# Kernel optimization log

Hardware: AMD Instinct MI355X
Metric: run time of the kernel (lower is better)

The kernel has to match this reference:

```python
import math
import jax, jax.numpy as jnp
import numpy as np

B, N, H, NH, DD, L = 4, 384, 256, 8, 32, 4
HD = H // NH
V = 11           # num_species + 1 (padding row 0)
CUTOFF = 5.0

def _ln(x, g, b):
    m = jnp.mean(x, axis=-1, keepdims=True)
    v = jnp.mean(jnp.square(x - m), axis=-1, keepdims=True)
    return (x - m) / jnp.sqrt(v + 1e-5) * g + b

def setup_inputs() -> dict:
    key = jax.random.key(0)
    ks = iter(jax.random.split(key, 64))
    def nrm(shape, s=0.05):
        return jax.random.normal(next(ks), shape, jnp.float32) * s
    return {
        'node_indices': jax.random.randint(next(ks), (B, N), 0, V),
        'positions': jax.random.normal(next(ks), (B, N, 3), jnp.float32),
        'mask': jnp.ones((B, N), jnp.float32),
        'emb': nrm((V, H)).at[0].set(0.0),
        'ln1_g': jnp.ones((L, H)), 'ln1_b': jnp.zeros((L, H)),
        'qkv_w': nrm((L, H, 3 * H)), 'qkv_b': jnp.zeros((L, 3 * H)),
        'out_w': nrm((L, H, H)), 'out_b': jnp.zeros((L, H)),
        'rb_w1': nrm((L, DD, H)), 'rb_b1': jnp.zeros((L, H)),
        'rb_w2': nrm((L, H, NH)), 'rb_b2': jnp.zeros((L, NH)),
        'gate_w1': nrm((L, H, H)), 'gate_b1': jnp.zeros((L, H)),
        'gate_w2': nrm((L, H, H)), 'gate_b2': jnp.zeros((L, H)),
        'ln2_g': jnp.ones((L, H)), 'ln2_b': jnp.zeros((L, H)),
        'ff_w1': nrm((L, H, 2 * H)), 'ff_b1': jnp.zeros((L, 2 * H)),
        'ff_w2': nrm((L, 2 * H, H)), 'ff_b2': jnp.zeros((L, H)),
        'pool_g': jnp.ones((H,)), 'pool_beta': jnp.zeros((H,)),
        'pool_w': nrm((H, H)), 'pool_b': jnp.zeros((H,)),
        'eh_w': nrm((H, 1)), 'eh_b': jnp.zeros((1,)),
    }

def _forward(node_indices, positions, mask, emb, ln1_g, ln1_b, qkv_w, qkv_b,
             out_w, out_b, rb_w1, rb_b1, rb_w2, rb_b2, gate_w1, gate_b1,
             gate_w2, gate_b2, ln2_g, ln2_b, ff_w1, ff_b1, ff_w2, ff_b2,
             pool_g, pool_beta, pool_w, pool_b, eh_w, eh_b):
    mask_b = mask > 0
    x = emb[node_indices] * mask_b[..., None]               # [B,N,H]
    pos = positions * mask_b[..., None].astype(positions.dtype)
    rel = pos[:, :, None, :] - pos[:, None, :, :]           # [B,N,N,3]
    dist = jnp.linalg.norm(rel + 1e-9, axis=-1)             # [B,N,N]
    adj = (dist <= CUTOFF).astype(jnp.float32)
    adj = adj * mask_b[:, None, :] * mask_b[:, :, None]
    edge = adj > 0
    isolated = mask_b & ~edge.any(axis=-1)
    adj = adj + isolated.astype(jnp.float32)[:, :, None] * jnp.eye(N, dtype=jnp.float32)
    edge = adj > 0
    # Bessel envelope features [B,N,N,DD]
    kk = jnp.arange(1, DD + 1, dtype=jnp.float32)
    ang = math.pi * kk * (dist / CUTOFF)[..., None]
    feat = jnp.sin(ang) / (dist[..., None] + 1e-6)
    feat = feat * (dist <= CUTOFF)[..., None].astype(jnp.float32)
    feat = feat * adj[..., None]

    scale = math.sqrt(HD)
    NEG = jnp.finfo(jnp.float32).min
    for l in range(L):
        res = x
        h = _ln(x, ln1_g[l], ln1_b[l])
        qkv = h @ qkv_w[l] + qkv_b[l]
        q, k, v = jnp.split(qkv, 3, axis=-1)
        q = q.reshape(B, N, NH, HD)
        k = k.reshape(B, N, NH, HD)
        v = v.reshape(B, N, NH, HD)
        logits = jnp.einsum('bihd,bjhd->bhij', q, k) / scale
        hb = jax.nn.silu(feat @ rb_w1[l] + rb_b1[l])        # [B,N,N,H]
        bias = hb @ rb_w2[l] + rb_b2[l]                     # [B,N,N,NH]
        logits = logits + bias.transpose(0, 3, 1, 2)
        logits = jnp.where(edge[:, None, :, :], logits, NEG)
        attn = jax.nn.softmax(logits, axis=-1)
        ctx = jnp.einsum('bhij,bjhd->bihd', attn, v).reshape(B, N, H)
        gated = jax.nn.silu(h @ gate_w1[l] + gate_b1[l]) @ gate_w2[l] + gate_b2[l]
        x = res + ((ctx * jax.nn.sigmoid(gated)) @ out_w[l] + out_b[l])
        y = _ln(x, ln2_g[l], ln2_b[l])
        x = x + (jax.nn.gelu(y @ ff_w1[l] + ff_b1[l], approximate=False) @ ff_w2[l] + ff_b2[l])

    pooled = jax.nn.silu(_ln(x, pool_g, pool_beta) @ pool_w + pool_b)
    masked = pooled * mask_b[..., None]
    counts = jnp.maximum(jnp.sum(mask_b, axis=1), 1)
    graph = jnp.sum(masked, axis=1) / counts[:, None]
    energy = (graph @ eh_w + eh_b)[:, 0]                    # [B]
    return energy

def reference(node_indices, positions, mask, emb, ln1_g, ln1_b, qkv_w, qkv_b,
              out_w, out_b, rb_w1, rb_b1, rb_w2, rb_b2, gate_w1, gate_b1,
              gate_w2, gate_b2, ln2_g, ln2_b, ff_w1, ff_b1, ff_w2, ff_b2,
              pool_g, pool_beta, pool_w, pool_b, eh_w, eh_b):
    return _forward(node_indices, positions, mask, emb, ln1_g, ln1_b, qkv_w,
                    qkv_b, out_w, out_b, rb_w1, rb_b1, rb_w2, rb_b2, gate_w1,
                    gate_b1, gate_w2, gate_b2, ln2_g, ln2_b, ff_w1, ff_b1,
                    ff_w2, ff_b2, pool_g, pool_beta, pool_w, pool_b, eh_w, eh_b)
```

## Files before the change

kernel.cpp:

```cpp
#include <hip/hip_runtime.h>
#include <hip/hip_bf16.h>
#include <math.h>

constexpr int B_ = 4, N_ = 384, H_ = 256, NH_ = 8, DD_ = 32, L_ = 4;
constexpr int M_ = B_ * N_;
constexpr float CUT = 5.0f;
constexpr float PI_ = 3.14159265358979323846f;
constexpr float INVSC = 0.17677669529663687f;
constexpr int TBL_N = 4096;
constexpr int TBL_STRIDE = 4098;

typedef __attribute__((ext_vector_type(8))) short short8;
typedef __attribute__((ext_vector_type(4))) float f32x4;
typedef __attribute__((ext_vector_type(4))) unsigned short u16x4;
using u16 = unsigned short;

__device__ __forceinline__ u16 f2b(float f) {
  __hip_bfloat16 h = __float2bfloat16(f);
  return *reinterpret_cast<u16*>(&h);
}
__device__ __forceinline__ float b2f(u16 u) {
  __hip_bfloat16 h;
  *reinterpret_cast<u16*>(&h) = u;
  return __bfloat162float(h);
}

__device__ __forceinline__ float wave_sum(float v) {
#pragma unroll
  for (int s = 1; s < 64; s <<= 1) v += __shfl_xor(v, s);
  return v;
}


__device__ __forceinline__ void bias_item(const float* __restrict__ pos,
                                          const float* __restrict__ mask,
                                          const float* __restrict__ tbl2,
                                          u16* __restrict__ biasb, int e) {
  int j = e % N_;
  int t = e / N_;
  int i = t % N_;
  int b = t / N_;
  float mi = mask[b * N_ + i], mj = mask[b * N_ + j];
  const float* pi = pos + (size_t)(b * N_ + i) * 3;
  const float* pj = pos + (size_t)(b * N_ + j) * 3;
  float dx = pi[0] - pj[0] + 1e-9f;
  float dy = pi[1] - pj[1] + 1e-9f;
  float dz = pi[2] - pj[2] + 1e-9f;
  float d = sqrtf(dx * dx + dy * dy + dz * dz);
  bool edge = (mi > 0.f && mj > 0.f) && (d <= CUT);
  size_t plane = (size_t)N_ * N_;
  size_t obase = (size_t)b * NH_ * plane + (size_t)i * N_ + j;
  size_t lstride = (size_t)B_ * NH_ * plane;
  if (edge) {
    int ixrow;
    float fr;
    if (i == j) {
      ixrow = TBL_N + 1;
      fr = 0.f;
    } else {
      float u = d * ((float)TBL_N / CUT);
      int ix = (int)u;
      ix = ix > TBL_N - 1 ? TBL_N - 1 : ix;
      fr = u - (float)ix;
      ixrow = ix;
    }
    const float4* r0 = (const float4*)(tbl2 + (size_t)ixrow * 32);
    const float4* r1 = (const float4*)(tbl2 + (size_t)(ixrow + 1) * 32);
    float4 a0[8], a1[8];
#pragma unroll
    for (int q = 0; q < 8; q++) {
      a0[q] = r0[q];
      a1[q] = r1[q];
    }
    float w0 = 1.f - fr;
#pragma unroll
    for (int q = 0; q < 8; q++) {
      float v0[4] = {a0[q].x, a0[q].y, a0[q].z, a0[q].w};
      float v1[4] = {a1[q].x, a1[q].y, a1[q].z, a1[q].w};
#pragma unroll
      for (int c = 0; c < 4; c++) {
        int lh = q * 4 + c;
        int l = lh >> 3, h = lh & 7;
        float v = v0[c] * w0 + v1[c] * fr;
        biasb[(size_t)l * lstride + obase + (size_t)h * plane] = f2b(v);
      }
    }
  } else {
#pragma unroll
    for (int lh = 0; lh < 32; lh++) {
      int l = lh >> 3, h = lh & 7;
      biasb[(size_t)l * lstride + obase + (size_t)h * plane] = 0xFF80;
    }
  }
}

struct TrJob {
  const float* src;
  u16* dst;
  int K, N, nx, ny, nz, base, dstride;
};
struct TrJobs {
  TrJob j[7];
};
__global__ __launch_bounds__(256) void setup_all_k(TrJobs jobs,
                                                   const float* __restrict__ rb_w1,
                                                   const float* __restrict__ rb_b1,
                                                   const float* __restrict__ rb_w2,
                                                   const float* __restrict__ rb_b2,
                                                   float* __restrict__ tbl2,
                                                   const int* __restrict__ nidx,
                                                   const float* __restrict__ mask,
                                                   const float* __restrict__ emb,
                                                   float* __restrict__ X) {
  __shared__ float sfA[64][32];
  __shared__ float hbA[64][260];
  __shared__ float t[32][33];
  int bid = blockIdx.x;
  int tid = threadIdx.x;
  if (bid < 260) {
    constexpr int TT = 64;
    int l = bid / 65;
    int t0 = (bid % 65) * TT;
#pragma unroll
    for (int m = 0; m < 8; m++) {
      int idx = m * 256 + tid;
      int tl = idx >> 5, k = idx & 31;
      int tt = t0 + tl;
      float d = (tt <= TBL_N) ? (tt * (CUT / (float)TBL_N)) : 1.7320508075688772e-9f;
      float ang = PI_ * (k + 1) * d * (1.f / CUT);
      sfA[tl][k] = sinf(ang) / (d + 1e-6f);
    }
    __syncthreads();
    float w1c[32];
    const float* w1 = rb_w1 + (size_t)l * DD_ * H_;
#pragma unroll
    for (int k = 0; k < 32; k++) w1c[k] = w1[k * H_ + tid];
    float b1v = rb_b1[l * H_ + tid];
    for (int tl = 0; tl < TT; tl++) {
      float pre = b1v;
      const float4* sfp = (const float4*)sfA[tl];
#pragma unroll
      for (int kq = 0; kq < 8; kq++) {
        float4 s4 = sfp[kq];
        pre += s4.x * w1c[kq * 4] + s4.y * w1c[kq * 4 + 1] + s4.z * w1c[kq * 4 + 2] +
               s4.w * w1c[kq * 4 + 3];
      }
      hbA[tl][tid] = pre / (1.f + __expf(-pre));
    }
    __syncthreads();
    const float* w2 = rb_w2 + (size_t)l * H_ * NH_;
    int o = tid & 7;
    float b2v = rb_b2[l * NH_ + o];
#pragma unroll
    for (int half = 0; half < 2; half++) {
      int tl = (tid >> 3) + half * 32;
      float acc = b2v;
      const float4* hp = (const float4*)hbA[tl];
#pragma unroll 4
      for (int hq = 0; hq < 64; hq++) {
        float4 h4 = hp[hq];
        acc += h4.x * w2[(hq * 4 + 0) * NH_ + o] + h4.y * w2[(hq * 4 + 1) * NH_ + o] +
               h4.z * w2[(hq * 4 + 2) * NH_ + o] + h4.w * w2[(hq * 4 + 3) * NH_ + o];
      }
      int tt = t0 + tl;
      if (tt <= TBL_STRIDE) tbl2[(size_t)tt * 32 + l * NH_ + o] = acc;
    }
  } else if (bid < 2884) {
    int tb = bid - 260;
    int ji = 0;
#pragma unroll
    for (int q = 1; q < 7; q++)
      if (tb >= jobs.j[q].base) ji = q;
    const TrJob& J = jobs.j[ji];
    int local = tb - J.base;
    int z = local / (J.nx * J.ny);
    int r2 = local % (J.nx * J.ny);
    int ky = r2 / J.nx, kx = r2 % J.nx;
    int n0 = kx * 32, k0 = ky * 32;
    const float* s = J.src + (size_t)z * J.K * J.N;
    u16* d = J.dst + (size_t)z * J.dstride;
    int r = tid >> 3, c4 = (tid & 7) * 4;
    float4 v = *(const float4*)(s + (size_t)(k0 + r) * J.N + n0 + c4);
    t[r][c4 + 0] = v.x;
    t[r][c4 + 1] = v.y;
    t[r][c4 + 2] = v.z;
    t[r][c4 + 3] = v.w;
    __syncthreads();
    u16x4 o;
    o[0] = f2b(t[c4 + 0][r]);
    o[1] = f2b(t[c4 + 1][r]);
    o[2] = f2b(t[c4 + 2][r]);
    o[3] = f2b(t[c4 + 3][r]);
    *(u16x4*)(d + (size_t)(n0 + r) * J.K + k0 + c4) = o;
  } else {
    int e = (bid - 2884) * 256 + tid;
    int mrow = e >> 8, c = e & 255;
    float mb = mask[mrow] > 0.f ? 1.f : 0.f;
    X[e] = emb[nidx[mrow] * H_ + c] * mb;
  }
}

__global__ __launch_bounds__(256) void ln_k(const float* __restrict__ X,
                                            const float* __restrict__ g,
                                            const float* __restrict__ bta,
                                            u16* __restrict__ O) {
  int wave = threadIdx.x >> 6, lane = threadIdx.x & 63;
  int row = blockIdx.x * 4 + wave;
  const float* xr = X + (size_t)row * H_;
  float4 v = *(const float4*)(xr + lane * 4);
  float s = v.x + v.y + v.z + v.w;
  s = wave_sum(s);
  float m = s * (1.f / H_);
  float dx = v.x - m, dy = v.y - m, dz = v.z - m, dw = v.w - m;
  float vs = dx * dx + dy * dy + dz * dz + dw * dw;
  vs = wave_sum(vs);
  float rs = rsqrtf(vs * (1.f / H_) + 1e-5f);
  float4 gg = *(const float4*)(g + lane * 4);
  float4 bb = *(const float4*)(bta + lane * 4);
  u16x4 o;
  o[0] = f2b(dx * rs * gg.x + bb.x);
  o[1] = f2b(dy * rs * gg.y + bb.y);
  o[2] = f2b(dz * rs * gg.z + bb.z);
  o[3] = f2b(dw * rs * gg.w + bb.w);
  *(u16x4*)(O + (size_t)row * H_ + lane * 4) = o;
}

template <int ACT, bool RES, bool PRE, bool OBF>
__device__ __forceinline__ void mgemm_body(u16* __restrict__ As, u16* __restrict__ Bs,
                                           const void* __restrict__ Av,
                                           const u16* __restrict__ WT,
                                           const float* __restrict__ bias,
                                           const float* __restrict__ resid,
                                           void* __restrict__ Cv, int K, int Nc,
                                           int lda, const float* __restrict__ G,
                                           const float* __restrict__ bias2,
                                           int m0, int n0) {
  const int tid = threadIdx.x;
  const int wave = tid >> 6, lane = tid & 63;
  const int wr = wave >> 1, wc = wave & 1, lr = lane & 15, lg = lane >> 4;
  f32x4 acc[2][2] = {};
  const int srow = tid >> 2, sp = tid & 3;
  for (int k0 = 0; k0 < K; k0 += 128) {
#pragma unroll
    for (int s4 = 0; s4 < 4; s4++) {
      int s = sp * 4 + s4;
      int phys = s ^ (srow & 15);
      if (PRE) {
        const float* ap = (const float*)Av + (size_t)(m0 + srow) * lda + k0 + s * 8;
        const float* gp = G + (size_t)(m0 + srow) * lda + k0 + s * 8;
        float4 a0 = *(const float4*)ap;
        float4 a1 = *(const float4*)(ap + 4);
        float4 g0 = *(const float4*)gp;
        float4 g1 = *(const float4*)(gp + 4);
        short8 vv;
        vv[0] = (short)f2b(a0.x / (1.f + __expf(-g0.x)));
        vv[1] = (short)f2b(a0.y / (1.f + __expf(-g0.y)));
        vv[2] = (short)f2b(a0.z / (1.f + __expf(-g0.z)));
        vv[3] = (short)f2b(a0.w / (1.f + __expf(-g0.w)));
        vv[4] = (short)f2b(a1.x / (1.f + __expf(-g1.x)));
        vv[5] = (short)f2b(a1.y / (1.f + __expf(-g1.y)));
        vv[6] = (short)f2b(a1.z / (1.f + __expf(-g1.z)));
        vv[7] = (short)f2b(a1.w / (1.f + __expf(-g1.w)));
        *(short8*)&As[srow * 128 + phys * 8] = vv;
      } else {
        const u16* Ab = (const u16*)Av;
        short8 v = *(const short8*)(Ab + (size_t)(m0 + srow) * lda + k0 + s * 8);
        *(short8*)&As[srow * 128 + phys * 8] = v;
      }
      short8 w = *(const short8*)(WT + (size_t)(n0 + srow) * K + k0 + s * 8);
      *(short8*)&Bs[srow * 128 + phys * 8] = w;
    }
    __syncthreads();
#pragma unroll
    for (int kk = 0; kk < 4; kk++) {
      int slot = kk * 4 + lg;
      short8 af[2], bf_[2];
#pragma unroll
      for (int i = 0; i < 2; i++) {
        int row = wr * 32 + i * 16 + lr;
        af[i] = *(const short8*)&As[row * 128 + (slot ^ (row & 15)) * 8];
      }
#pragma unroll
      for (int j = 0; j < 2; j++) {
        int row = wc * 32 + j * 16 + lr;
        bf_[j] = *(const short8*)&Bs[row * 128 + (slot ^ (row & 15)) * 8];
      }
#pragma unroll
      for (int i = 0; i < 2; i++)
#pragma unroll
        for (int j = 0; j < 2; j++)
          acc[i][j] = __builtin_amdgcn_mfma_f32_16x16x32_bf16(af[i], bf_[j], acc[i][j], 0, 0, 0);
    }
    __syncthreads();
  }
#pragma unroll
  for (int i = 0; i < 2; i++)
#pragma unroll
    for (int j = 0; j < 2; j++)
#pragma unroll
      for (int rg = 0; rg < 4; rg++) {
        int row = m0 + wr * 32 + i * 16 + lg * 4 + rg;
        int col = n0 + wc * 32 + j * 16 + lr;
        float v;
        if (ACT == 3) {
          float bv = (col < 768) ? bias[col] : bias2[col - 768];
          v = acc[i][j][rg] + bv;
          if (col >= 768) v = v / (1.f + __expf(-v));
        } else {
          v = acc[i][j][rg] + bias[col];
          if (ACT == 1) v = v / (1.f + __expf(-v));
          if (ACT == 2) v = 0.5f * v * (1.f + erff(v * 0.70710678118654752f));
        }
        if (RES) v += resid[(size_t)row * Nc + col];
        if (OBF)
          ((u16*)Cv)[(size_t)row * Nc + col] = f2b(v);
        else
          ((float*)Cv)[(size_t)row * Nc + col] = v;
      }
}

template <int ACT, bool RES, bool PRE, bool OBF>
__global__ __launch_bounds__(256) void mgemm_k(const void* __restrict__ Av,
                                               const u16* __restrict__ WT,
                                               const float* __restrict__ bias,
                                               const float* __restrict__ resid,
                                               void* __restrict__ Cv, int K, int Nc,
                                               int lda, const float* __restrict__ G,
                                               const float* __restrict__ bias2) {
  __shared__ u16 As[64 * 128];
  __shared__ u16 Bs[64 * 128];
  mgemm_body<ACT, RES, PRE, OBF>(As, Bs, Av, WT, bias, resid, Cv, K, Nc, lda, G, bias2,
                                 blockIdx.y * 64, blockIdx.x * 64);
}

__global__ __launch_bounds__(256) void qkv_bias_k(const u16* __restrict__ hb,
                                                  const u16* __restrict__ wqg,
                                                  const float* __restrict__ qb,
                                                  const float* __restrict__ gb1,
                                                  u16* __restrict__ qgb,
                                                  const float* __restrict__ pos,
                                                  const float* __restrict__ mask,
                                                  const float* __restrict__ tbl2,
                                                  u16* __restrict__ biasb) {
  __shared__ u16 As[64 * 128];
  __shared__ u16 Bs[64 * 128];
  int bid = blockIdx.x;
  if (bid < 384) {
    mgemm_body<3, false, false, true>(As, Bs, hb, wqg, qb, nullptr, qgb, 256, 1024, 256,
                                      nullptr, gb1, (bid >> 4) * 64, (bid & 15) * 64);
  } else {
    bias_item(pos, mask, tbl2, biasb, (bid - 384) * 256 + threadIdx.x);
  }
}

__device__ __forceinline__ void attn_body(u16* __restrict__ FragQ, u16* __restrict__ FragK,
                                          u16* __restrict__ FragV, float* __restrict__ smax,
                                          float* __restrict__ ssum,
                                          const u16* __restrict__ qkv,
                                          const u16* __restrict__ biasb,
                                          float* __restrict__ ctx, int qs,
                                          int it, int hh, int b) {
  u16* FragP = FragK;
  float* pbuf = (float*)FragV;
  const int i0 = it * 32;
  const int tid = threadIdx.x;
  const size_t bb = (size_t)b * N_;

  if (tid < 128) {
    int q = tid >> 2, dc = tid & 3;
    short8 v = *(const short8*)(qkv + (bb + i0 + q) * qs + hh * 32 + dc * 8);
    *(short8*)&FragQ[(((q >> 4) * 64) + (q & 15) + 16 * dc) * 8] = v;
  }
#pragma unroll
  for (int m = 0; m < 6; m++) {
    int idx = m * 256 + tid;
    int key = idx >> 2, dc = idx & 3;
    const u16* kb = qkv + (bb + key) * qs + 256 + hh * 32 + dc * 8;
    short8 kv = *(const short8*)kb;
    *(short8*)&FragK[(((key >> 4) * 64) + (key & 15) + 16 * dc) * 8] = kv;
    short8 vv = *(const short8*)(kb + 256);
    int kc = key >> 5, sub = (key >> 3) & 3, kj = key & 7;
#pragma unroll
    for (int j = 0; j < 8; j++) {
      int d = dc * 8 + j;
      FragV[(((kc * 2 + (d >> 4)) * 64) + (d & 15) + 16 * sub) * 8 + kj] = (u16)vv[j];
    }
  }
  __syncthreads();

  const int wave = tid >> 6, lane = tid & 63;
  const int rh = wave & 1, kh = wave >> 1;
  const int g = lane >> 4, c = lane & 15;
  const u16* bptr = biasb + (size_t)(b * NH_ + hh) * N_ * N_;

  short8 qf = *(const short8*)&FragQ[(rh * 64 + lane) * 8];
  f32x4 sc[12];
#pragma unroll
  for (int t = 0; t < 12; t++) {
    int T = kh * 12 + t;
    short8 kf = *(const short8*)&FragK[(T * 64 + lane) * 8];
    f32x4 z = {0.f, 0.f, 0.f, 0.f};
    sc[t] = __builtin_amdgcn_mfma_f32_16x16x32_bf16(qf, kf, z, 0, 0, 0);
    int key = 16 * T + c;
#pragma unroll
    for (int reg = 0; reg < 4; reg++) {
      int row = i0 + 16 * rh + 4 * g + reg;
      float bv = b2f(bptr[(size_t)row * N_ + key]);
      sc[t][reg] = sc[t][reg] * INVSC + bv;
    }
  }
  float mx[4];
#pragma unroll
  for (int reg = 0; reg < 4; reg++) {
    float m = sc[0][reg];
#pragma unroll
    for (int t = 1; t < 12; t++) m = fmaxf(m, sc[t][reg]);
#pragma unroll
    for (int s = 1; s < 16; s <<= 1) m = fmaxf(m, __shfl_xor(m, s));
    mx[reg] = m;
  }
  if (c == 0) {
#pragma unroll
    for (int reg = 0; reg < 4; reg++) smax[kh * 32 + 16 * rh + 4 * g + reg] = mx[reg];
  }
  __syncthreads();
  float sm[4];
#pragma unroll
  for (int reg = 0; reg < 4; reg++) {
    float M = fmaxf(smax[16 * rh + 4 * g + reg], smax[32 + 16 * rh + 4 * g + reg]);
    float s = 0.f;
#pragma unroll
    for (int t = 0; t < 12; t++) {
      float p = __expf(sc[t][reg] - M);
      sc[t][reg] = p;
      s += p;
    }
    sm[reg] = s;
  }
#pragma unroll
  for (int reg = 0; reg < 4; reg++) {
#pragma unroll
    for (int s = 1; s < 16; s <<= 1) sm[reg] += __shfl_xor(sm[reg], s);
  }
  if (c == 0) {
#pragma unroll
    for (int reg = 0; reg < 4; reg++) ssum[kh * 32 + 16 * rh + 4 * g + reg] = sm[reg];
  }
#pragma unroll
  for (int t = 0; t < 12; t++) {
    int T = kh * 12 + t;
    int kc = T >> 1;
    int sub = (2 * T + (c >> 3)) & 3;
#pragma unroll
    for (int reg = 0; reg < 4; reg++) {
      FragP[((rh * 12 + kc) * 64 + (4 * g + reg) + 16 * sub) * 8 + (c & 7)] =
          f2b(sc[t][reg]);
    }
  }
  __syncthreads();
  float Ls[4];
#pragma unroll
  for (int reg = 0; reg < 4; reg++)
    Ls[reg] = ssum[16 * rh + 4 * g + reg] + ssum[32 + 16 * rh + 4 * g + reg];

  f32x4 pcc[2] = {};
#pragma unroll
  for (int t = 0; t < 6; t++) {
    int kc = kh * 6 + t;
    short8 pf = *(const short8*)&FragP[((rh * 12 + kc) * 64 + lane) * 8];
#pragma unroll
    for (int nh = 0; nh < 2; nh++) {
      short8 vf = *(const short8*)&FragV[((kc * 2 + nh) * 64 + lane) * 8];
      pcc[nh] = __builtin_amdgcn_mfma_f32_16x16x32_bf16(pf, vf, pcc[nh], 0, 0, 0);
    }
  }
  __syncthreads();
  if (kh == 1) {
#pragma unroll
    for (int nh = 0; nh < 2; nh++)
#pragma unroll
      for (int reg = 0; reg < 4; reg++)
        pbuf[rh * 512 + (4 * g + reg) * 32 + nh * 16 + c] = pcc[nh][reg];
  }
  __syncthreads();
  if (kh == 0) {
#pragma unroll
    for (int nh = 0; nh < 2; nh++)
#pragma unroll
      for (int reg = 0; reg < 4; reg++) {
        float v = pcc[nh][reg] + pbuf[rh * 512 + (4 * g + reg) * 32 + nh * 16 + c];
        int row = i0 + 16 * rh + 4 * g + reg;
        ctx[(bb + row) * H_ + hh * 32 + nh * 16 + c] = v / Ls[reg];
      }
  }
}

__global__ __launch_bounds__(256) void attn_g2_k(const u16* __restrict__ qkv,
                                                 const u16* __restrict__ biasb,
                                                 float* __restrict__ ctx,
                                                 const u16* __restrict__ wg2,
                                                 const float* __restrict__ gb2,
                                                 float* __restrict__ g2) {
  __shared__ __align__(16) u16 SMEM[(2 + 24 + 24) * 64 * 8];
  __shared__ float sred[2 * 32 * 2];
  int bid = blockIdx.x;
  if (bid < 384) {
    int it = bid % 12;
    int t = bid / 12;
    attn_body(SMEM, SMEM + 1024, SMEM + 1024 + 12288, sred, sred + 64,
              qkv, biasb, ctx, 1024, it, t % NH_, t / NH_);
  } else {
    int g = bid - 384;
    mgemm_body<0, false, false, false>(SMEM, SMEM + 8192, (const void*)(qkv + 768), wg2,
                                       gb2, nullptr, g2, 256, 256, 1024, nullptr,
                                       nullptr, (g >> 2) * 64, (g & 3) * 64);
  }
}

__global__ __launch_bounds__(256) void energy_k(const float* __restrict__ p2,
                                                const float* __restrict__ mask,
                                                const float* __restrict__ ehw,
                                                const float* __restrict__ ehb,
                                                float* __restrict__ out) {
  int b = blockIdx.x, h = threadIdx.x;
  float s = 0.f, cnt = 0.f;
#pragma unroll 4
  for (int i = 0; i < N_; i++) {
    float m = mask[b * N_ + i] > 0.f ? 1.f : 0.f;
    s += p2[(size_t)(b * N_ + i) * H_ + h] * m;
    cnt += m;
  }
  float val = s * ehw[h];
  __shared__ float red[256];
  red[h] = val;
  __syncthreads();
  for (int st = 128; st > 0; st >>= 1) {
    if (h < st) red[h] += red[h + st];
    __syncthreads();
  }
  if (h == 0) {
    float c = cnt < 1.f ? 1.f : cnt;
    out[b] = red[0] / c + ehb[0];
  }
}

extern "C" void kernel_launch(void* const* d_in, const int* in_sizes, int n_in,
                              void* d_out, int out_size, void* d_ws, size_t ws_size,
                              hipStream_t stream) {
  const int* node_idx = (const int*)d_in[0];
  const float* positions = (const float*)d_in[1];
  const float* mask = (const float*)d_in[2];
  const float* emb = (const float*)d_in[3];
  const float* ln1_g = (const float*)d_in[4];
  const float* ln1_b = (const float*)d_in[5];
  const float* qkv_w = (const float*)d_in[6];
  const float* qkv_b = (const float*)d_in[7];
  const float* out_w = (const float*)d_in[8];
  const float* out_b = (const float*)d_in[9];
  const float* rb_w1 = (const float*)d_in[10];
  const float* rb_b1 = (const float*)d_in[11];
  const float* rb_w2 = (const float*)d_in[12];
  const float* rb_b2 = (const float*)d_in[13];
  const float* gate_w1 = (const float*)d_in[14];
  const float* gate_b1 = (const float*)d_in[15];
  const float* gate_w2 = (const float*)d_in[16];
  const float* gate_b2 = (const float*)d_in[17];
  const float* ln2_g = (const float*)d_in[18];
  const float* ln2_b = (const float*)d_in[19];
  const float* ff_w1 = (const float*)d_in[20];
  const float* ff_b1 = (const float*)d_in[21];
  const float* ff_w2 = (const float*)d_in[22];
  const float* ff_b2 = (const float*)d_in[23];
  const float* pool_g = (const float*)d_in[24];
  const float* pool_beta = (const float*)d_in[25];
  const float* pool_w = (const float*)d_in[26];
  const float* pool_b = (const float*)d_in[27];
  const float* eh_w = (const float*)d_in[28];
  const float* eh_b = (const float*)d_in[29];
  float* eout = (float*)d_out;

  char* W8 = (char*)d_ws;
  float* x = (float*)(W8 + 0);
  u16* qgb = (u16*)(W8 + 1572864);
  float* ctx = (float*)(W8 + 4718592);
  float* g2 = (float*)(W8 + 6291456);
  u16* hb = (u16*)(W8 + 7864320);
  u16* ffb = (u16*)(W8 + 8650752);
  float* tbl2 = (float*)(W8 + 12582912);
  u16* wt = (u16*)(W8 + 13631488);
  u16* wt_qg = wt;
  u16* wt_out = wt + 1048576;
  u16* wt_g2 = wt + 1310720;
  u16* wt_f1 = wt + 1572864;
  u16* wt_f2 = wt + 2097152;
  u16* wt_p = wt + 2621440;
  u16* biasb = (u16*)(W8 + 19005440);
  const size_t bias_lstride = (size_t)B_ * NH_ * N_ * N_;

  {
    TrJobs jobs;
    jobs.j[0] = {qkv_w, wt_qg, 256, 768, 24, 8, 4, 0, 262144};
    jobs.j[1] = {gate_w1, wt_qg + 768 * 256, 256, 256, 8, 8, 4, 768, 262144};
    jobs.j[2] = {out_w, wt_out, 256, 256, 8, 8, 4, 1024, 65536};
    jobs.j[3] = {gate_w2, wt_g2, 256, 256, 8, 8, 4, 1280, 65536};
    jobs.j[4] = {ff_w1, wt_f1, 256, 512, 16, 8, 4, 1536, 131072};
    jobs.j[5] = {ff_w2, wt_f2, 512, 256, 8, 16, 4, 2048, 131072};
    jobs.j[6] = {pool_w, wt_p, 256, 256, 8, 8, 1, 2560, 65536};
    setup_all_k<<<4420, 256, 0, stream>>>(jobs, rb_w1, rb_b1, rb_w2, rb_b2, tbl2,
                                          node_idx, mask, emb, x);
  }

  for (int l = 0; l < L_; l++) {
    const float* qb = qkv_b + (size_t)l * 3 * H_;
    const float* ob = out_b + (size_t)l * H_;
    const float* gb1 = gate_b1 + (size_t)l * H_;
    const float* gb2 = gate_b2 + (size_t)l * H_;
    const float* fb1 = ff_b1 + (size_t)l * 2 * H_;
    const float* fb2 = ff_b2 + (size_t)l * H_;
    u16* wqg = wt_qg + (size_t)l * 1024 * 256;
    u16* wo = wt_out + (size_t)l * 256 * 256;
    u16* wg2 = wt_g2 + (size_t)l * 256 * 256;
    u16* wf1 = wt_f1 + (size_t)l * 512 * 256;
    u16* wf2 = wt_f2 + (size_t)l * 256 * 512;

    ln_k<<<M_ / 4, 256, 0, stream>>>(x, ln1_g + l * H_, ln1_b + l * H_, hb);
    if (l == 0) {
      qkv_bias_k<<<2688, 256, 0, stream>>>(hb, wqg, qb, gb1, qgb, positions, mask, tbl2,
                                           biasb);
    } else {
      mgemm_k<3, false, false, true><<<dim3(16, 24), 256, 0, stream>>>(
          hb, wqg, qb, nullptr, qgb, 256, 1024, 256, nullptr, gb1);
    }
    attn_g2_k<<<480, 256, 0, stream>>>(qgb, biasb + (size_t)l * bias_lstride, ctx,
                                       wg2, gb2, g2);
    mgemm_k<0, true, true, false><<<dim3(4, 24), 256, 0, stream>>>(
        ctx, wo, ob, x, x, 256, 256, 256, g2, nullptr);
    ln_k<<<M_ / 4, 256, 0, stream>>>(x, ln2_g + l * H_, ln2_b + l * H_, hb);
    mgemm_k<2, false, false, true><<<dim3(8, 24), 256, 0, stream>>>(
        hb, wf1, fb1, nullptr, ffb, 256, 512, 256, nullptr, nullptr);
    mgemm_k<0, true, false, false><<<dim3(4, 24), 256, 0, stream>>>(
        ffb, wf2, fb2, x, x, 512, 256, 512, nullptr, nullptr);
  }

  ln_k<<<M_ / 4, 256, 0, stream>>>(x, pool_g, pool_beta, hb);
  mgemm_k<1, false, false, false><<<dim3(4, 24), 256, 0, stream>>>(
      hb, wt_p, pool_b, nullptr, ctx, 256, 256, 256, nullptr, nullptr);
  energy_k<<<B_, 256, 0, stream>>>(ctx, mask, eh_w, eh_b, eout);
}
```

Before: 275.9 us.

## Fuse LayerNorm into residual GEMM epilogues and embedding setup

Removes the standalone LayerNorm kernels. The first LN is folded into the embedding branch of the setup kernel. Each later LN runs in the epilogue of a new full-row GEMM kernel (64 rows × 256 cols per block) that handles the out-projection and FF2 residual updates. This saves several launches and a re-read of x per layer. In exchange, these GEMMs now launch only 24 blocks instead of 96, which cuts parallelism on a large GPU. Variance is computed as E[x²]−mean² in one pass, which is less numerically stable than the two-pass form.

```diff
diff --git a/kernel.cpp b/kernel.cpp
--- a/kernel.cpp
+++ b/kernel.cpp
@@ -111,10 +111,14 @@
                                                    const int* __restrict__ nidx,
                                                    const float* __restrict__ mask,
                                                    const float* __restrict__ emb,
-                                                   float* __restrict__ X) {
+                                                   float* __restrict__ X,
+                                                   const float* __restrict__ l1g,
+                                                   const float* __restrict__ l1b,
+                                                   u16* __restrict__ HB) {
   __shared__ float sfA[64][32];
   __shared__ float hbA[64][260];
   __shared__ float t[32][33];
+  __shared__ float sw[8];
   int bid = blockIdx.x;
   int tid = threadIdx.x;
   if (bid < 260) {
@@ -193,36 +197,24 @@
     o[3] = f2b(t[c4 + 3][r]);
     *(u16x4*)(d + (size_t)(n0 + r) * J.K + k0 + c4) = o;
   } else {
-    int e = (bid - 2884) * 256 + tid;
-    int mrow = e >> 8, c = e & 255;
-    float mb = mask[mrow] > 0.f ? 1.f : 0.f;
-    X[e] = emb[nidx[mrow] * H_ + c] * mb;
-  }
-}
-
-__global__ __launch_bounds__(256) void ln_k(const float* __restrict__ X,
-                                            const float* __restrict__ g,
-                                            const float* __restrict__ bta,
-                                            u16* __restrict__ O) {
-  int wave = threadIdx.x >> 6, lane = threadIdx.x & 63;
-  int row = blockIdx.x * 4 + wave;
-  const float* xr = X + (size_t)row * H_;
-  float4 v = *(const float4*)(xr + lane * 4);
-  float s = v.x + v.y + v.z + v.w;
-  s = wave_sum(s);
-  float m = s * (1.f / H_);
-  float dx = v.x - m, dy = v.y - m, dz = v.z - m, dw = v.w - m;
-  float vs = dx * dx + dy * dy + dz * dz + dw * dw;
-  vs = wave_sum(vs);
-  float rs = rsqrtf(vs * (1.f / H_) + 1e-5f);
-  float4 gg = *(const float4*)(g + lane * 4);
-  float4 bb = *(const float4*)(bta + lane * 4);
-  u16x4 o;
-  o[0] = f2b(dx * rs * gg.x + bb.x);
-  o[1] = f2b(dy * rs * gg.y + bb.y);
-  o[2] = f2b(dz * rs * gg.z + bb.z);
-  o[3] = f2b(dw * rs * gg.w + bb.w);
-  *(u16x4*)(O + (size_t)row * H_ + lane * 4) = o;
+    int row = bid - 2884;
+    float mb = mask[row] > 0.f ? 1.f : 0.f;
+    float v = emb[nidx[row] * H_ + tid] * mb;
+    X[(size_t)row * H_ + tid] = v;
+    float s = wave_sum(v);
+    float q = wave_sum(v * v);
+    int wv = tid >> 6, ln = tid & 63;
+    if (ln == 0) {
+      sw[wv] = s;
+      sw[4 + wv] = q;
+    }
+    __syncthreads();
+    float ts = sw[0] + sw[1] + sw[2] + sw[3];
+    float tq = sw[4] + sw[5] + sw[6] + sw[7];
+    float m = ts * (1.f / 256.f);
+    float rs = rsqrtf(tq * (1.f / 256.f) - m * m + 1e-5f);
+    HB[(size_t)row * H_ + tid] = f2b((v - m) * rs * l1g[tid] + l1b[tid]);
+  }
 }
 
 template <int ACT, bool RES, bool PRE, bool OBF>
@@ -331,6 +323,114 @@
   __shared__ u16 Bs[64 * 128];
   mgemm_body<ACT, RES, PRE, OBF>(As, Bs, Av, WT, bias, resid, Cv, K, Nc, lda, G, bias2,
                                  blockIdx.y * 64, blockIdx.x * 64);
+}
+
+template <bool PRE>
+__global__ __launch_bounds__(256) void glngemm_k(const void* __restrict__ Av,
+                                                 const u16* __restrict__ WT,
+                                                 const float* __restrict__ bias,
+                                                 const float* __restrict__ G,
+                                                 float* __restrict__ Xio,
+                                                 u16* __restrict__ hb,
+                                                 const float* __restrict__ lng,
+                                                 const float* __restrict__ lnb,
+                                                 int K, int lda) {
+  __shared__ u16 As[64 * 64];
+  __shared__ u16 Bs[256 * 64];
+  const int m0 = blockIdx.x * 64;
+  const int tid = threadIdx.x;
+  const int wave = tid >> 6, lane = tid & 63;
+  const int lr = lane & 15, lg = lane >> 4;
+  f32x4 acc[16] = {};
+  const int srow = tid >> 2, sp = tid & 3;
+  for (int k0 = 0; k0 < K; k0 += 64) {
+#pragma unroll
+    for (int s2 = 0; s2 < 2; s2++) {
+      int s = sp * 2 + s2;
+      int phys = s ^ (srow & 7);
+      if (PRE) {
+        const float* ap = (const float*)Av + (size_t)(m0 + srow) * lda + k0 + s * 8;
+        const float* gp = G + (size_t)(m0 + srow) * lda + k0 + s * 8;
+        short8 vv;
+#pragma unroll
+        for (int q = 0; q < 8; q++) {
+          vv[q] = (short)f2b(ap[q] / (1.f + __expf(-gp[q])));
+        }
+        *(short8*)&As[srow * 64 + phys * 8] = vv;
+      } else {
+        short8 v = *(const short8*)((const u16*)Av + (size_t)(m0 + srow) * lda + k0 + s * 8);
+        *(short8*)&As[srow * 64 + phys * 8] = v;
+      }
+    }
+    {
+      const u16* wr_ = WT + (size_t)tid * K + k0;
+#pragma unroll
+      for (int s = 0; s < 8; s++) {
+        int phys = s ^ (tid & 7);
+        *(short8*)&Bs[tid * 64 + phys * 8] = *(const short8*)(wr_ + s * 8);
+      }
+    }
+    __syncthreads();
+#pragma unroll
+    for (int grp = 0; grp < 2; grp++) {
+      int arow = wave * 16 + lr;
+      int achunk = (grp * 4 + lg) ^ (arow & 7);
+      short8 af = *(const short8*)&As[arow * 64 + achunk * 8];
+#pragma unroll
+      for (int t = 0; t < 16; t++) {
+        int brow = t * 16 + lr;
+        int bchunk = (grp * 4 + lg) ^ (brow & 7);
+        short8 bf = *(const short8*)&Bs[brow * 64 + bchunk * 8];
+        acc[t] = __builtin_amdgcn_mfma_f32_16x16x32_bf16(af, bf, acc[t], 0, 0, 0);
+      }
+    }
+    __syncthreads();
+  }
+#pragma unroll
+  for (int t = 0; t < 16; t++) {
+    int col = t * 16 + lr;
+    float bv = bias[col];
+#pragma unroll
+    for (int reg = 0; reg < 4; reg++) {
+      int row = m0 + wave * 16 + lg * 4 + reg;
+      float v = acc[t][reg] + bv + Xio[(size_t)row * 256 + col];
+      acc[t][reg] = v;
+      Xio[(size_t)row * 256 + col] = v;
+    }
+  }
+  float sum[4] = {}, sq[4] = {};
+#pragma unroll
+  for (int t = 0; t < 16; t++)
+#pragma unroll
+    for (int reg = 0; reg < 4; reg++) {
+      float v = acc[t][reg];
+      sum[reg] += v;
+      sq[reg] += v * v;
+    }
+#pragma unroll
+  for (int reg = 0; reg < 4; reg++) {
+#pragma unroll
+    for (int s = 1; s < 16; s <<= 1) {
+      sum[reg] += __shfl_xor(sum[reg], s);
+      sq[reg] += __shfl_xor(sq[reg], s);
+    }
+  }
+  float mean[4], rstd[4];
+#pragma unroll
+  for (int reg = 0; reg < 4; reg++) {
+    mean[reg] = sum[reg] * (1.f / 256.f);
+    rstd[reg] = rsqrtf(sq[reg] * (1.f / 256.f) - mean[reg] * mean[reg] + 1e-5f);
+  }
+#pragma unroll
+  for (int t = 0; t < 16; t++) {
+    int col = t * 16 + lr;
+    float gg = lng[col], bb = lnb[col];
+#pragma unroll
+    for (int reg = 0; reg < 4; reg++) {
+      int row = m0 + wave * 16 + lg * 4 + reg;
+      hb[(size_t)row * 256 + col] = f2b((acc[t][reg] - mean[reg]) * rstd[reg] * gg + bb);
+    }
+  }
 }
 
 __global__ __launch_bounds__(256) void qkv_bias_k(const u16* __restrict__ hb,
@@ -607,7 +707,7 @@
     jobs.j[5] = {ff_w2, wt_f2, 512, 256, 8, 16, 4, 2048, 131072};
     jobs.j[6] = {pool_w, wt_p, 256, 256, 8, 8, 1, 2560, 65536};
     setup_all_k<<<4420, 256, 0, stream>>>(jobs, rb_w1, rb_b1, rb_w2, rb_b2, tbl2,
-                                          node_idx, mask, emb, x);
+                                          node_idx, mask, emb, x, ln1_g, ln1_b, hb);
   }
 
   for (int l = 0; l < L_; l++) {
@@ -623,7 +723,6 @@
     u16* wf1 = wt_f1 + (size_t)l * 512 * 256;
     u16* wf2 = wt_f2 + (size_t)l * 256 * 512;
 
-    ln_k<<<M_ / 4, 256, 0, stream>>>(x, ln1_g + l * H_, ln1_b + l * H_, hb);
     if (l == 0) {
       qkv_bias_k<<<2688, 256, 0, stream>>>(hb, wqg, qb, gb1, qgb, positions, mask, tbl2,
                                            biasb);
@@ -633,16 +732,16 @@
     }
     attn_g2_k<<<480, 256, 0, stream>>>(qgb, biasb + (size_t)l * bias_lstride, ctx,
                                        wg2, gb2, g2);
-    mgemm_k<0, true, true, false><<<dim3(4, 24), 256, 0, stream>>>(
-        ctx, wo, ob, x, x, 256, 256, 256, g2, nullptr);
-    ln_k<<<M_ / 4, 256, 0, stream>>>(x, ln2_g + l * H_, ln2_b + l * H_, hb);
+    glngemm_k<true><<<24, 256, 0, stream>>>(ctx, wo, ob, g2, x, hb,
+                                            ln2_g + l * H_, ln2_b + l * H_, 256, 256);
     mgemm_k<2, false, false, true><<<dim3(8, 24), 256, 0, stream>>>(
         hb, wf1, fb1, nullptr, ffb, 256, 512, 256, nullptr, nullptr);
-    mgemm_k<0, true, false, false><<<dim3(4, 24), 256, 0, stream>>>(
-        ffb, wf2, fb2, x, x, 512, 256, 512, nullptr, nullptr);
-  }
-
-  ln_k<<<M_ / 4, 256, 0, stream>>>(x, pool_g, pool_beta, hb);
+    const float* nlg = (l < 3) ? (ln1_g + (l + 1) * H_) : pool_g;
+    const float* nlb = (l < 3) ? (ln1_b + (l + 1) * H_) : pool_beta;
+    glngemm_k<false><<<24, 256, 0, stream>>>(ffb, wf2, fb2, nullptr, x, hb,
+                                             nlg, nlb, 512, 512);
+  }
+
   mgemm_k<1, false, false, false><<<dim3(4, 24), 256, 0, stream>>>(
       hb, wt_p, pool_b, nullptr, ctx, 256, 256, 256, nullptr, nullptr);
   energy_k<<<B_, 256, 0, stream>>>(ctx, mask, eh_w, eh_b, eout);
```

Result: slower. 356.9 us (+29.3%).
